# Kernel tuning notes

Measured on AMD Instinct MI355X. Metric: run time of the kernel, lower is better.

## Reference

```python
import jax, jax.numpy as jnp
import numpy as np

B, L, D_MODEL, HEADS, EXP, DEPTH = 2, 2048, 1024, 16, 2, 12
D_EXP = D_MODEL * EXP
D_HEAD = D_EXP // HEADS


def _layernorm(x, g, b, eps=1e-5):
    mu = jnp.mean(x, axis=-1, keepdims=True)
    var = jnp.mean(jnp.square(x - mu), axis=-1, keepdims=True)
    return (x - mu) * jax.lax.rsqrt(var + eps) * g + b


def setup_inputs() -> dict:
    key = jax.random.key(0)
    ks = jax.random.split(key, 4)
    x = jax.random.normal(ks[0], (B, L, D_MODEL), dtype=jnp.float32)
    w_in = jax.random.normal(ks[1], (D_MODEL, 4 * D_EXP), dtype=jnp.float32) * 0.02
    w_out = jax.random.normal(ks[2], (D_EXP, D_MODEL), dtype=jnp.float32) * (0.02 / np.sqrt(2 * DEPTH))
    return {
        "x": x,
        "ln1_g": jnp.ones((D_MODEL,), jnp.float32),
        "ln1_b": jnp.zeros((D_MODEL,), jnp.float32),
        "ln2_g": jnp.ones((D_MODEL,), jnp.float32),
        "ln2_b": jnp.zeros((D_MODEL,), jnp.float32),
        "w_in": w_in,
        "w_out": w_out,
        "smear_factor": jnp.linspace(-6.0, 6.0, HEADS, dtype=jnp.float32),
        "log_scale": jnp.zeros((HEADS,), jnp.float32),
    }


def reference(x, ln1_g, ln1_b, ln2_g, ln2_b, w_in, w_out, smear_factor, log_scale):
    b, l, d = x.shape
    h = smear_factor.shape[0]
    d_exp = w_in.shape[1] // 4
    dh = d_exp // h

    qkvp = _layernorm(x, ln1_g, ln1_b) @ w_in  # [b, l, 4*d_exp]
    q, k, v, p = jnp.split(qkvp, 4, axis=-1)
    # 'b i (h d) -> b h i d'
    to_heads = lambda t: t.reshape(b, l, h, dh).transpose(0, 2, 1, 3)
    q, k, v = to_heads(q), to_heads(k), to_heads(v)

    # smeared keys: k_i <- (1-s)*k_i + s*k_{i-1}  (zero at i=0)
    smear = jax.nn.sigmoid(smear_factor)[None, :, None, None]
    k_prev = jnp.pad(k, ((0, 0), (0, 0), (1, 0), (0, 0)))[:, :, :-1, :]
    k = (1.0 - smear) * k + smear * k_prev

    # ALiBi-style additive mask: slope[h]*j on causal part, -1e10 above diag
    half = h // 2
    slopes = jnp.concatenate([2.0 ** jnp.linspace(0.0, -8.0, half), jnp.zeros((h - half,), jnp.float32)])
    j = jnp.arange(l)
    causal = jnp.where(j[None, :] > j[:, None], jnp.float32(-1e10), jnp.float32(0.0))  # [l, l]
    mask = slopes[:, None, None] * j[None, None, :].astype(jnp.float32) + causal[None, :, :]  # [h, l, l]

    # SDPA with q/s, k/s and default scale 1/sqrt(dh): logits = q k^T / (s^2 sqrt(dh))
    inv = 1.0 / (jnp.exp(2.0 * log_scale)[None, :, None, None] * jnp.sqrt(jnp.float32(dh)))
    logits = jnp.einsum('bhid,bhjd->bhij', q, k) * inv + mask[None]
    attn = jax.nn.softmax(logits, axis=-1)
    o = jnp.einsum('bhij,bhjd->bhid', attn, v)
    o = o.transpose(0, 2, 1, 3).reshape(b, l, h * dh)  # 'b h i d -> b i (h d)'

    out = (jax.nn.silu(p) * o) @ w_out
    return _layernorm(out, ln2_g, ln2_b)
```

## Files before the change

kernel.cpp:

```cpp
#include <hip/hip_runtime.h>

typedef unsigned short u16;
typedef __attribute__((ext_vector_type(8))) short bf16x8;
typedef __attribute__((ext_vector_type(8))) unsigned short u16x8;
typedef __attribute__((ext_vector_type(4))) float f32x4;

#define L_SEQ 2048
#define NTOK 4096
#define DMODEL 1024
#define DEXP 2048
#define NH 16
#define DH 128

__device__ __forceinline__ u16 f2bf(float f) {
    unsigned u = __float_as_uint(f);
    unsigned r = (u + 0x7FFFu + ((u >> 16) & 1u)) >> 16;
    return (u16)r;
}
__device__ __forceinline__ float bf2f(u16 h) {
    return __uint_as_float(((unsigned)h) << 16);
}

__device__ __forceinline__ void gl_lds16(const u16* g, u16* l) {
    __builtin_amdgcn_global_load_lds((const __attribute__((address_space(1))) void*)g,
                                     (__attribute__((address_space(3))) void*)l, 16, 0, 0);
}

__global__ void conv_transpose(const float* __restrict__ in, u16* __restrict__ out, int R, int C) {
    __shared__ unsigned tile[32][33];
    int c0 = blockIdx.x * 32, r0 = blockIdx.y * 32;
    int tx = threadIdx.x, ty = threadIdx.y;
    for (int j = 0; j < 32; j += 8)
        tile[ty + j][tx] = (unsigned)f2bf(in[(size_t)(r0 + ty + j) * C + c0 + tx]);
    __syncthreads();
    for (int j = 0; j < 32; j += 8)
        out[(size_t)(c0 + ty + j) * R + r0 + tx] = (u16)tile[tx][ty + j];
}

__global__ __launch_bounds__(256) void ln_fwd(const float* __restrict__ x, const float* __restrict__ g,
                                              const float* __restrict__ bta, void* __restrict__ outp,
                                              int out_bf16) {
    int row = blockIdx.x;
    int t = threadIdx.x;
    const float* xr = x + (size_t)row * DMODEL;
    float4 xv = *(const float4*)&xr[t * 4];
    float s = xv.x + xv.y + xv.z + xv.w;
    float s2 = xv.x * xv.x + xv.y * xv.y + xv.z * xv.z + xv.w * xv.w;
    for (int off = 32; off >= 1; off >>= 1) {
        s += __shfl_xor(s, off);
        s2 += __shfl_xor(s2, off);
    }
    __shared__ float red[10];
    int w = t >> 6;
    if ((t & 63) == 0) { red[w] = s; red[4 + w] = s2; }
    __syncthreads();
    if (t == 0) {
        red[8] = red[0] + red[1] + red[2] + red[3];
        red[9] = red[4] + red[5] + red[6] + red[7];
    }
    __syncthreads();
    float mu = red[8] * (1.0f / DMODEL);
    float var = red[9] * (1.0f / DMODEL) - mu * mu;
    float rstd = rsqrtf(var + 1e-5f);
    float vals[4] = {xv.x, xv.y, xv.z, xv.w};
    for (int e = 0; e < 4; e++) {
        int c = t * 4 + e;
        float y = (vals[e] - mu) * rstd * g[c] + bta[c];
        if (out_bf16) ((u16*)outp)[(size_t)row * DMODEL + c] = f2bf(y);
        else          ((float*)outp)[(size_t)row * DMODEL + c] = y;
    }
}

__device__ __forceinline__ void store_out(u16* C, size_t idx, float v) { C[idx] = f2bf(v); }
__device__ __forceinline__ void store_out(float* C, size_t idx, float v) { C[idx] = v; }

template <typename OutT>
__global__ __launch_bounds__(256) void gemm_bt(const u16* __restrict__ A, const u16* __restrict__ BT,
                                               OutT* __restrict__ C, int M, int N, int K) {
    __shared__ u16 a_s[2][4096];
    __shared__ u16 b_s[2][4096];
    int tid = threadIdx.x;
    unsigned NX = gridDim.x;
    unsigned lin = blockIdx.x + NX * blockIdx.y;
    unsigned per = NX >> 3;
    unsigned xcd = lin & 7, t = lin >> 3;
    unsigned n_p = xcd * per + (t % per);
    unsigned m_p = t / per;
    int m0 = m_p * 128, n0 = n_p * 128;
    int w = tid >> 6, lane = tid & 63, quad = lane >> 4, ln = lane & 15;
    int wr = (w >> 1) * 64, wc = (w & 1) * 64;
    f32x4 zero4 = {0.f, 0.f, 0.f, 0.f};
    f32x4 acc[4][4];
    for (int r = 0; r < 4; r++)
        for (int c = 0; c < 4; c++) acc[r][c] = zero4;

    int lrow = lane >> 2;
    int lseg = ((lane & 3) ^ ((lrow >> 1) & 3)) * 8;
    int qsw = (quad ^ ((ln >> 1) & 3)) * 8;
    const u16* Ag0 = A + (size_t)(m0 + 32 * w + lrow) * K + lseg;
    const u16* Ag1 = Ag0 + (size_t)16 * K;
    const u16* Bg0 = BT + (size_t)(n0 + 32 * w + lrow) * K + lseg;
    const u16* Bg1 = Bg0 + (size_t)16 * K;
    int lo0 = (2 * w) * 512, lo1 = (2 * w + 1) * 512;

    gl_lds16(Ag0, &a_s[0][lo0]);
    gl_lds16(Ag1, &a_s[0][lo1]);
    gl_lds16(Bg0, &b_s[0][lo0]);
    gl_lds16(Bg1, &b_s[0][lo1]);
    __syncthreads();

    int cur = 0;
    for (int k0 = 0; k0 < K; k0 += 32) {
        if (k0 + 32 < K) {
            int nb = cur ^ 1;
            gl_lds16(Ag0 + k0 + 32, &a_s[nb][lo0]);
            gl_lds16(Ag1 + k0 + 32, &a_s[nb][lo1]);
            gl_lds16(Bg0 + k0 + 32, &b_s[nb][lo0]);
            gl_lds16(Bg1 + k0 + 32, &b_s[nb][lo1]);
        }
        bf16x8 af[4], bfr[4];
        for (int r = 0; r < 4; r++) af[r]  = *(const bf16x8*)&a_s[cur][(wr + r * 16 + ln) * 32 + qsw];
        for (int c = 0; c < 4; c++) bfr[c] = *(const bf16x8*)&b_s[cur][(wc + c * 16 + ln) * 32 + qsw];
        __builtin_amdgcn_s_setprio(1);
        for (int r = 0; r < 4; r++)
            for (int c = 0; c < 4; c++)
                acc[r][c] = __builtin_amdgcn_mfma_f32_16x16x32_bf16(af[r], bfr[c], acc[r][c], 0, 0, 0);
        __builtin_amdgcn_s_setprio(0);
        __syncthreads();
        cur ^= 1;
    }
    for (int r = 0; r < 4; r++)
        for (int c = 0; c < 4; c++)
            for (int e = 0; e < 4; e++) {
                int row = m0 + wr + r * 16 + quad * 4 + e;
                int col = n0 + wc + c * 16 + ln;
                store_out(C, (size_t)row * N + col, acc[r][c][e]);
            }
}

__global__ __launch_bounds__(256) void smear_kernel(const u16* __restrict__ qkvp,
                                                    const float* __restrict__ smear_f,
                                                    u16* __restrict__ k_sm) {
    int gid = blockIdx.x * 256 + threadIdx.x;
    int base = gid * 8;
    int bl = base >> 11;
    int c = base & 2047;
    int h = c >> 7;
    int d = c & 127;
    int l = bl & (L_SEQ - 1);
    int bb = bl >> 11;
    float s = 1.0f / (1.0f + __expf(-smear_f[h]));
    u16x8 cur = *(const u16x8*)&qkvp[(size_t)bl * 8192 + 2048 + c];
    u16x8 prv = {0, 0, 0, 0, 0, 0, 0, 0};
    if (l > 0) prv = *(const u16x8*)&qkvp[(size_t)(bl - 1) * 8192 + 2048 + c];
    u16x8 outv;
    for (int u = 0; u < 8; u++) {
        float kc = bf2f(cur[u]);
        float kp = bf2f(prv[u]);
        outv[u] = f2bf((1.0f - s) * kc + s * kp);
    }
    *(u16x8*)&k_sm[(((size_t)(bb * 16 + h)) * L_SEQ + l) * DH + d] = outv;
}

__global__ void vT_kernel(const u16* __restrict__ qkvp, u16* __restrict__ v_t) {
    __shared__ unsigned tile[32][33];
    int l0 = blockIdx.x * 32, d0 = blockIdx.y * 32;
    int bh = blockIdx.z;
    int bb = bh >> 4, h = bh & 15;
    int tx = threadIdx.x, ty = threadIdx.y;
    size_t tokb = (size_t)bb * L_SEQ;
    for (int j = 0; j < 32; j += 8)
        tile[ty + j][tx] = (unsigned)qkvp[(tokb + l0 + ty + j) * 8192 + 4096 + h * DH + d0 + tx];
    __syncthreads();
    for (int j = 0; j < 32; j += 8)
        v_t[((size_t)bh * DH + d0 + ty + j) * L_SEQ + l0 + tx] = (u16)tile[tx][ty + j];
}

__global__ __launch_bounds__(256) void attn_kernel(const u16* __restrict__ qkvp,
                                                   const u16* __restrict__ k_sm,
                                                   const u16* __restrict__ v_t,
                                                   u16* __restrict__ ag2,
                                                   const float* __restrict__ log_scale) {
    __shared__ u16 k_s[16384];
    __shared__ u16 vt_s[16384];
    __shared__ u16 p_s[4608];
    int tid = threadIdx.x;
    unsigned lin = blockIdx.x + 16u * blockIdx.y;
    unsigned xcd = lin & 7, tt = lin >> 3;
    int bh = (int)(xcd * 4 + (tt & 3));
    int pair = (int)(tt >> 2);
    int bb = bh >> 4, h = bh & 15;
    int w = tid >> 6, lane = tid & 63, quad = lane >> 4, ln = lane & 15;
    size_t tokb = (size_t)bb * L_SEQ;

    const float LOG2E = 1.44269504f;
    float inv = 1.0f / (__expf(2.0f * log_scale[h]) * sqrtf((float)DH));
    float scl = inv * LOG2E;
    float slope2 = ((h < 8) ? exp2f(-8.0f * (float)h / 7.0f) : 0.0f) * LOG2E;

    int lrow = lane >> 2, lcol = lane & 3;
    int lsw8 = (lcol ^ ((lrow >> 1) & 3)) * 8;
    int qsw = (quad ^ ((ln >> 1) & 3)) * 8;
    f32x4 zero4 = {0.f, 0.f, 0.f, 0.f};
    u16* pw = &p_s[w * 1152];
    const short ONE_BF = (short)0x3F80;
    bf16x8 ones = {ONE_BF, ONE_BF, ONE_BF, ONE_BF, ONE_BF, ONE_BF, ONE_BF, ONE_BF};

    for (int sidx = 0; sidx < 2; sidx++) {
        int ib = sidx == 0 ? (31 - pair) : pair;
        int i0 = ib * 64;
        int si = i0 + w * 16;
        int iq = si + ln;

        bf16x8 qf[4];
        for (int kt = 0; kt < 4; kt++)
            qf[kt] = *(const bf16x8*)&qkvp[(tokb + si + ln) * 8192 + h * DH + kt * 32 + quad * 8];

        float m_i = -1e30f;
        f32x4 o_acc[8], l_acc;
        for (int dt = 0; dt < 8; dt++) o_acc[dt] = zero4;
        l_acc = zero4;

        float adt[4][4];
        for (int ct = 0; ct < 4; ct++)
            for (int r = 0; r < 4; r++)
                adt[ct][r] = slope2 * (float)(ct * 16 + quad * 4 + r);
        float astep = slope2 * 64.0f;

        const u16* kg[4];
        for (int g = 0; g < 4; g++)
            kg[g] = k_sm + ((size_t)bh * L_SEQ + g * 16 + lrow) * DH + w * 32 + lsw8;
        const u16* vg[4];
        int vloff[4];
        for (int q = 0; q < 4; q++) {
            int c = w * 4 + q;
            int jt = c >> 3, dg = c & 7;
            vg[q] = v_t + ((size_t)bh * DH + dg * 16 + lrow) * L_SEQ + jt * 32 + lsw8;
            vloff[q] = jt * 4096 + dg * 512;
        }

        for (int g = 0; g < 4; g++) { gl_lds16(kg[g], &k_s[w * 2048 + g * 512]); kg[g] += 64 * DH; }
        for (int q = 0; q < 4; q++) { gl_lds16(vg[q], &vt_s[vloff[q]]); vg[q] += 64; }
        __syncthreads();

        int cur = 0;
        for (int j0 = 0; j0 <= i0; j0 += 64) {
            if (j0 + 64 <= i0) {
                int nb = (cur ^ 1) * 8192;
                for (int g = 0; g < 4; g++) { gl_lds16(kg[g], &k_s[nb + w * 2048 + g * 512]); kg[g] += 64 * DH; }
                for (int q = 0; q < 4; q++) { gl_lds16(vg[q], &vt_s[nb + vloff[q]]); vg[q] += 64; }
            }
            const u16* kb = &k_s[cur * 8192];
            const u16* vb = &vt_s[cur * 8192];

            f32x4 sc[4];
            for (int ct = 0; ct < 4; ct++) sc[ct] = zero4;
            __builtin_amdgcn_s_setprio(1);
            for (int kt = 0; kt < 4; kt++)
                for (int ct = 0; ct < 4; ct++) {
                    bf16x8 bfr = *(const bf16x8*)&kb[kt * 2048 + (ct * 16 + ln) * 32 + qsw];
                    sc[ct] = __builtin_amdgcn_mfma_f32_16x16x32_bf16(bfr, qf[kt], sc[ct], 0, 0, 0);
                }
            __builtin_amdgcn_s_setprio(0);

            bool full = (j0 + 63 <= si);
            float s2[4][4];
            for (int ct = 0; ct < 4; ct++)
                for (int r = 0; r < 4; r++) {
                    float v = fmaf(sc[ct][r], scl, adt[ct][r]);
                    if (!full) {
                        int j = j0 + ct * 16 + quad * 4 + r;
                        if (j > iq) v = -3.0e38f;
                    }
                    s2[ct][r] = v;
                }
            float mr = s2[0][0];
            for (int ct = 0; ct < 4; ct++)
                for (int r = 0; r < 4; r++) mr = fmaxf(mr, s2[ct][r]);
            mr = fmaxf(mr, __shfl_xor(mr, 16));
            mr = fmaxf(mr, __shfl_xor(mr, 32));
            float mnew = fmaxf(m_i, mr);
            float alpha = exp2f(m_i - mnew);
            m_i = mnew;

            for (int ct = 0; ct < 4; ct++) {
                float p0 = exp2f(s2[ct][0] - mnew);
                float p1 = exp2f(s2[ct][1] - mnew);
                float p2 = exp2f(s2[ct][2] - mnew);
                float p3 = exp2f(s2[ct][3] - mnew);
                unsigned d0 = (__float_as_uint(p1) & 0xFFFF0000u) | (__float_as_uint(p0) >> 16);
                unsigned d1 = (__float_as_uint(p3) & 0xFFFF0000u) | (__float_as_uint(p2) >> 16);
                uint2 dd; dd.x = d0; dd.y = d1;
                *(uint2*)&pw[ln * 72 + ct * 16 + quad * 4] = dd;
            }
            for (int ct = 0; ct < 4; ct++)
                for (int r = 0; r < 4; r++) adt[ct][r] += astep;

            if (__any(alpha != 1.0f)) {
                float av[4];
                for (int e = 0; e < 4; e++) av[e] = __shfl(alpha, quad * 20 + e);
                for (int dt = 0; dt < 8; dt++) {
                    f32x4 o = o_acc[dt];
                    for (int e = 0; e < 4; e++) o[e] *= av[e];
                    o_acc[dt] = o;
                }
                for (int e = 0; e < 4; e++) l_acc[e] *= av[e];
            }
            asm volatile("s_waitcnt lgkmcnt(0)" ::: "memory");
            __builtin_amdgcn_s_setprio(1);
            for (int ks = 0; ks < 2; ks++) {
                bf16x8 pa = *(const bf16x8*)&pw[ln * 72 + ks * 32 + quad * 8];
                l_acc = __builtin_amdgcn_mfma_f32_16x16x32_bf16(pa, ones, l_acc, 0, 0, 0);
                for (int dt = 0; dt < 8; dt++) {
                    bf16x8 vf = *(const bf16x8*)&vb[ks * 4096 + (dt * 16 + ln) * 32 + qsw];
                    o_acc[dt] = __builtin_amdgcn_mfma_f32_16x16x32_bf16(pa, vf, o_acc[dt], 0, 0, 0);
                }
            }
            __builtin_amdgcn_s_setprio(0);
            __syncthreads();
            cur ^= 1;
        }

        float rinv[4];
        for (int r = 0; r < 4; r++) rinv[r] = __builtin_amdgcn_rcpf(l_acc[r]);
        for (int dt = 0; dt < 8; dt++)
            for (int r = 0; r < 4; r++) {
                int i = si + quad * 4 + r;
                int dcol = dt * 16 + ln;
                float o = o_acc[dt][r] * rinv[r];
                float pv = bf2f(qkvp[(tokb + i) * 8192 + 6144 + h * DH + dcol]);
                float gate = pv * __builtin_amdgcn_rcpf(1.0f + exp2f(-pv * LOG2E));
                ag2[(tokb + i) * 2048 + h * DH + dcol] = f2bf(gate * o);
            }
    }
}

extern "C" void kernel_launch(void* const* d_in, const int* in_sizes, int n_in,
                              void* d_out, int out_size, void* d_ws, size_t ws_size,
                              hipStream_t stream) {
    const float* x       = (const float*)d_in[0];
    const float* ln1_g   = (const float*)d_in[1];
    const float* ln1_b   = (const float*)d_in[2];
    const float* ln2_g   = (const float*)d_in[3];
    const float* ln2_b   = (const float*)d_in[4];
    const float* w_in    = (const float*)d_in[5];
    const float* w_out   = (const float*)d_in[6];
    const float* smear_f = (const float*)d_in[7];
    const float* logsc   = (const float*)d_in[8];
    float* out = (float*)d_out;
    char* ws = (char*)d_ws;

    u16* w_inT   = (u16*)(ws + 0);
    u16* w_outT  = (u16*)(ws + (size_t)16777216);
    u16* lnA     = (u16*)(ws + (size_t)20971520);
    u16* qkvp    = (u16*)(ws + (size_t)29360128);
    u16* k_sm    = (u16*)(ws + (size_t)96468992);
    u16* ag2     = (u16*)(ws + (size_t)113246208);
    float* out_pre = (float*)(ws + (size_t)96468992);
    u16* v_t     = (u16*)(ws + 0);

    dim3 b32x8(32, 8);
    conv_transpose<<<dim3(8192 / 32, 1024 / 32), b32x8, 0, stream>>>(w_in, w_inT, 1024, 8192);
    conv_transpose<<<dim3(1024 / 32, 2048 / 32), b32x8, 0, stream>>>(w_out, w_outT, 2048, 1024);
    ln_fwd<<<NTOK, 256, 0, stream>>>(x, ln1_g, ln1_b, (void*)lnA, 1);
    gemm_bt<u16><<<dim3(8192 / 128, 4096 / 128), 256, 0, stream>>>(lnA, w_inT, qkvp, NTOK, 8192, 1024);
    smear_kernel<<<4096, 256, 0, stream>>>(qkvp, smear_f, k_sm);
    vT_kernel<<<dim3(L_SEQ / 32, DH / 32, 32), b32x8, 0, stream>>>(qkvp, v_t);
    attn_kernel<<<dim3(16, 32), 256, 0, stream>>>(qkvp, k_sm, v_t, ag2, logsc);
    gemm_bt<float><<<dim3(1024 / 128, 4096 / 128), 256, 0, stream>>>(ag2, w_outT, out_pre, NTOK, 1024, 2048);
    ln_fwd<<<NTOK, 256, 0, stream>>>(out_pre, ln2_g, ln2_b, (void*)out, 0);
}
```

Before: 355.7 us.

## Add 64-row tile GEMM for output projection and trim attention softmax ops

Adds a gemm_bt64 kernel that uses 64x128 tiles with an XCD-aware block remap and uses it for the output projection. The smaller tiles double the block count (256 to 512) so the 256 CUs stay busier. In attention, the per-element ALiBi bias increment is replaced by shifting the running max by the slope step each tile, which is equivalent since the bias grows uniformly. The attention change also uses a tree max reduction and v_perm to pack bf16. The smaller tiles cost less operand reuse per block, and the shifted-max trick slightly changes floating-point rounding.

```diff
diff --git a/kernel.cpp b/kernel.cpp
--- a/kernel.cpp
+++ b/kernel.cpp
@@ -135,6 +135,67 @@
                 int row = m0 + wr + r * 16 + quad * 4 + e;
                 int col = n0 + wc + c * 16 + ln;
                 store_out(C, (size_t)row * N + col, acc[r][c][e]);
+            }
+}
+
+__global__ __launch_bounds__(256) void gemm_bt64(const u16* __restrict__ A, const u16* __restrict__ BT,
+                                                 float* __restrict__ C, int M, int N, int K) {
+    __shared__ u16 a_s[2][2048];
+    __shared__ u16 b_s[2][4096];
+    int tid = threadIdx.x;
+    unsigned NX = gridDim.x;
+    unsigned lin = blockIdx.x + NX * blockIdx.y;
+    unsigned per = NX >> 3;
+    unsigned xcd = lin & 7, t = lin >> 3;
+    unsigned n_p = xcd * per + (t % per);
+    unsigned m_p = t / per;
+    int m0 = m_p * 64, n0 = n_p * 128;
+    int w = tid >> 6, lane = tid & 63, quad = lane >> 4, ln = lane & 15;
+    int wc = w * 32;
+    f32x4 zero4 = {0.f, 0.f, 0.f, 0.f};
+    f32x4 acc[4][2];
+    for (int r = 0; r < 4; r++)
+        for (int c = 0; c < 2; c++) acc[r][c] = zero4;
+
+    int lrow = lane >> 2;
+    int lseg = ((lane & 3) ^ ((lrow >> 1) & 3)) * 8;
+    int qsw = (quad ^ ((ln >> 1) & 3)) * 8;
+    const u16* Ag  = A + (size_t)(m0 + 16 * w + lrow) * K + lseg;
+    const u16* Bg0 = BT + (size_t)(n0 + 32 * w + lrow) * K + lseg;
+    const u16* Bg1 = Bg0 + (size_t)16 * K;
+    int la = w * 512;
+    int lb0 = (2 * w) * 512, lb1 = (2 * w + 1) * 512;
+
+    gl_lds16(Ag, &a_s[0][la]);
+    gl_lds16(Bg0, &b_s[0][lb0]);
+    gl_lds16(Bg1, &b_s[0][lb1]);
+    __syncthreads();
+
+    int cur = 0;
+    for (int k0 = 0; k0 < K; k0 += 32) {
+        if (k0 + 32 < K) {
+            int nb = cur ^ 1;
+            gl_lds16(Ag + k0 + 32, &a_s[nb][la]);
+            gl_lds16(Bg0 + k0 + 32, &b_s[nb][lb0]);
+            gl_lds16(Bg1 + k0 + 32, &b_s[nb][lb1]);
+        }
+        bf16x8 af[4], bfr[2];
+        for (int r = 0; r < 4; r++) af[r]  = *(const bf16x8*)&a_s[cur][(r * 16 + ln) * 32 + qsw];
+        for (int c = 0; c < 2; c++) bfr[c] = *(const bf16x8*)&b_s[cur][(wc + c * 16 + ln) * 32 + qsw];
+        __builtin_amdgcn_s_setprio(1);
+        for (int r = 0; r < 4; r++)
+            for (int c = 0; c < 2; c++)
+                acc[r][c] = __builtin_amdgcn_mfma_f32_16x16x32_bf16(af[r], bfr[c], acc[r][c], 0, 0, 0);
+        __builtin_amdgcn_s_setprio(0);
+        __syncthreads();
+        cur ^= 1;
+    }
+    for (int r = 0; r < 4; r++)
+        for (int c = 0; c < 2; c++)
+            for (int e = 0; e < 4; e++) {
+                int row = m0 + r * 16 + quad * 4 + e;
+                int col = n0 + wc + c * 16 + ln;
+                C[(size_t)row * N + col] = acc[r][c][e];
             }
 }
 
@@ -216,16 +277,16 @@
         for (int kt = 0; kt < 4; kt++)
             qf[kt] = *(const bf16x8*)&qkvp[(tokb + si + ln) * 8192 + h * DH + kt * 32 + quad * 8];
 
-        float m_i = -1e30f;
+        float mshift = -1e30f;
+        float astep = slope2 * 64.0f;
         f32x4 o_acc[8], l_acc;
         for (int dt = 0; dt < 8; dt++) o_acc[dt] = zero4;
         l_acc = zero4;
 
-        float adt[4][4];
+        float adt0[4][4];
         for (int ct = 0; ct < 4; ct++)
             for (int r = 0; r < 4; r++)
-                adt[ct][r] = slope2 * (float)(ct * 16 + quad * 4 + r);
-        float astep = slope2 * 64.0f;
+                adt0[ct][r] = slope2 * (float)(ct * 16 + quad * 4 + r);
 
         const u16* kg[4];
         for (int g = 0; g < 4; g++)
@@ -267,34 +328,38 @@
             float s2[4][4];
             for (int ct = 0; ct < 4; ct++)
                 for (int r = 0; r < 4; r++) {
-                    float v = fmaf(sc[ct][r], scl, adt[ct][r]);
+                    float v = fmaf(sc[ct][r], scl, adt0[ct][r]);
                     if (!full) {
                         int j = j0 + ct * 16 + quad * 4 + r;
                         if (j > iq) v = -3.0e38f;
                     }
                     s2[ct][r] = v;
                 }
-            float mr = s2[0][0];
-            for (int ct = 0; ct < 4; ct++)
-                for (int r = 0; r < 4; r++) mr = fmaxf(mr, s2[ct][r]);
+            float x0 = fmaxf(fmaxf(s2[0][0], s2[0][1]), s2[0][2]);
+            float x1 = fmaxf(fmaxf(s2[0][3], s2[1][0]), s2[1][1]);
+            float x2 = fmaxf(fmaxf(s2[1][2], s2[1][3]), s2[2][0]);
+            float x3 = fmaxf(fmaxf(s2[2][1], s2[2][2]), s2[2][3]);
+            float x4 = fmaxf(fmaxf(s2[3][0], s2[3][1]), s2[3][2]);
+            float y0 = fmaxf(fmaxf(x0, x1), x2);
+            float y1 = fmaxf(fmaxf(x3, x4), s2[3][3]);
+            float mr = fmaxf(y0, y1);
             mr = fmaxf(mr, __shfl_xor(mr, 16));
             mr = fmaxf(mr, __shfl_xor(mr, 32));
-            float mnew = fmaxf(m_i, mr);
-            float alpha = exp2f(m_i - mnew);
-            m_i = mnew;
+            float msh_old = mshift - astep;
+            float mnew = fmaxf(msh_old, mr);
+            float alpha = exp2f(msh_old - mnew);
+            mshift = mnew;
 
             for (int ct = 0; ct < 4; ct++) {
                 float p0 = exp2f(s2[ct][0] - mnew);
                 float p1 = exp2f(s2[ct][1] - mnew);
                 float p2 = exp2f(s2[ct][2] - mnew);
                 float p3 = exp2f(s2[ct][3] - mnew);
-                unsigned d0 = (__float_as_uint(p1) & 0xFFFF0000u) | (__float_as_uint(p0) >> 16);
-                unsigned d1 = (__float_as_uint(p3) & 0xFFFF0000u) | (__float_as_uint(p2) >> 16);
+                unsigned d0 = __builtin_amdgcn_perm(__float_as_uint(p1), __float_as_uint(p0), 0x07060302u);
+                unsigned d1 = __builtin_amdgcn_perm(__float_as_uint(p3), __float_as_uint(p2), 0x07060302u);
                 uint2 dd; dd.x = d0; dd.y = d1;
                 *(uint2*)&pw[ln * 72 + ct * 16 + quad * 4] = dd;
             }
-            for (int ct = 0; ct < 4; ct++)
-                for (int r = 0; r < 4; r++) adt[ct][r] += astep;
 
             if (__any(alpha != 1.0f)) {
                 float av[4];
@@ -367,6 +432,6 @@
     smear_kernel<<<4096, 256, 0, stream>>>(qkvp, smear_f, k_sm);
     vT_kernel<<<dim3(L_SEQ / 32, DH / 32, 32), b32x8, 0, stream>>>(qkvp, v_t);
     attn_kernel<<<dim3(16, 32), 256, 0, stream>>>(qkvp, k_sm, v_t, ag2, logsc);
-    gemm_bt<float><<<dim3(1024 / 128, 4096 / 128), 256, 0, stream>>>(ag2, w_outT, out_pre, NTOK, 1024, 2048);
+    gemm_bt64<<<dim3(1024 / 128, 4096 / 64), 256, 0, stream>>>(ag2, w_outT, out_pre, NTOK, 1024, 2048);
     ln_fwd<<<NTOK, 256, 0, stream>>>(out_pre, ln2_g, ln2_b, (void*)out, 0);
 }
```

Result: faster. 346.0 us (-2.7%).
